# Kernel tuning notes

Hardware: AMD Instinct MI355X
Metric: run time of the kernel (lower is better)

Reference implementation:

```python
import jax, jax.numpy as jnp
import numpy as np

NUM_STEPS = 16  # step_index values in [0, 16); step 0 is excluded from pooling
BETA = 0.1
EPS = 1e-8


def setup_inputs() -> dict:
    key = jax.random.key(0)
    k1, k2, k3, k4, k5 = jax.random.split(key, 5)
    B, N, T, H, D = 8, 8, 2048, 2048, 1
    return {
        "policy_responses_logps": jax.random.normal(k1, (B, N, T, D), dtype=jnp.float32),
        "reference_responses_logps": jax.random.normal(k2, (B, N, T, D), dtype=jnp.float32),
        "hidden_state": jax.random.normal(k3, (B, N, T, H), dtype=jnp.float32),
        "step_index": jax.random.randint(k4, (B, N, T), 0, NUM_STEPS, dtype=jnp.int32),
        "labels": jax.random.normal(k5, (B, N), dtype=jnp.float32),
    }


def _segment_stats(onehot, x, counts):
    # onehot: [B,N,T,S], x: [B,N,T,F] -> per-step mean [B,N,S,F]
    ssum = jnp.einsum('bnts,bntf->bnsf', onehot, x)
    return ssum / jnp.maximum(counts, 1.0)[..., None]


def _lambda_rank_loss(pred, labels):
    # pred, labels: [B,N]
    N = pred.shape[1]
    diff = pred[:, :, None] - pred[:, None, :]            # [B,N,N]
    label_diff = labels[:, :, None] - labels[:, None, :]
    pairwise = -jax.nn.log_sigmoid(diff * jnp.sign(label_diff))
    return (pairwise.sum(axis=(1, 2)) / (N * (N - 1))).mean()


def reference(policy_responses_logps, reference_responses_logps, hidden_state, step_index, labels):
    logits = policy_responses_logps - reference_responses_logps  # [B,N,T,D]

    onehot = jax.nn.one_hot(step_index, NUM_STEPS, dtype=hidden_state.dtype)  # [B,N,T,S]
    counts = onehot.sum(axis=2)                                               # [B,N,S]

    step_hidden = _segment_stats(onehot, hidden_state, counts)  # [B,N,S,H]
    ref_hidden = step_hidden[:, 0:1]                             # [B,1,S,H]

    # cosine similarity between each (b,n,s) step-mean and the reference (n=0) step-mean
    dot = jnp.einsum('bnsh,bosh->bns', step_hidden, ref_hidden)
    nrm = jnp.maximum(jnp.linalg.norm(step_hidden, axis=-1), EPS)        # [B,N,S]
    ref_nrm = jnp.maximum(jnp.linalg.norm(ref_hidden, axis=-1), EPS)      # [B,1,S]
    cos = dot / (nrm * ref_nrm)

    s_ids = jnp.arange(NUM_STEPS)
    valid = (counts > 0) & (counts[:, 0:1] > 0) & (s_ids >= 1)[None, None, :]
    step_weights = jnp.where(valid, cos + 1.0, 0.0)                        # [B,N,S]

    step_logit = _segment_stats(onehot, logits, counts)                    # [B,N,S,D]
    weighted_sum = jnp.einsum('bns,bnsd->bnd', step_weights, step_logit)
    total_weight = step_weights.sum(axis=-1)                               # [B,N]
    weighted_logits = jnp.where(total_weight[..., None] > 0,
                                weighted_sum / jnp.maximum(total_weight, EPS)[..., None],
                                0.0)                                       # [B,N,D]

    text_logits = weighted_logits.mean(axis=-1)                            # [B,N]
    lr = _lambda_rank_loss(text_logits, labels)
    loss = -jax.nn.log_sigmoid(BETA * lr)

    chosen_rewards = (policy_responses_logps[:, 0, :] - reference_responses_logps[:, 0, :]).mean()
    rejected_rewards = (policy_responses_logps[:, -1, :] - reference_responses_logps[:, -1, :]).mean()
    return (loss, chosen_rewards, rejected_rewards)
```

## Files before the change

### kernel.cpp

```cpp
#include <hip/hip_runtime.h>
#include <math.h>

#define TT 2048
#define HH 2048
#define NSTEP 16
#define EPSF 1e-8f
#define BETA 0.1f
#define TSPLIT 2
#define TCHUNK (TT / TSPLIT)
#define ROW2 (HH / 2)
#define PART_FLOATS ((size_t)64 * NSTEP * HH)

typedef float f2v __attribute__((ext_vector_type(2)));

__global__ __launch_bounds__(256, 4) void k_segsum2(const float* __restrict__ hidden,
                                                    const int* __restrict__ step,
                                                    float2* __restrict__ part) {
  const int bn   = blockIdx.y;
  const int z    = blockIdx.z;
  const int col2 = blockIdx.x * 256 + threadIdx.x;
  const int t0   = z * TCHUNK;

  __shared__ int s_step[TCHUNK];
  for (int i = threadIdx.x; i < TCHUNK; i += 256) s_step[i] = step[bn * TT + t0 + i];
  __syncthreads();

  const f2v* hp = (const f2v*)hidden + (size_t)(bn * TT + t0) * ROW2 + col2;

  float2 acc[NSTEP];
#pragma unroll
  for (int k = 0; k < NSTEP; ++k) acc[k] = make_float2(0.f, 0.f);

  f2v va[8], vb[8];
  int4 sa0, sa1, sb0, sb1;

#define LOADS(S0, S1, base)                         \
  { S0 = *(const int4*)&s_step[(base)];             \
    S1 = *(const int4*)&s_step[(base) + 4]; }

#define LOADG(dst, base)                                        \
  _Pragma("unroll")                                             \
  for (int u = 0; u < 8; ++u)                                   \
    dst[u] = __builtin_nontemporal_load(&hp[(size_t)((base) + u) * ROW2]);

#define ACC1(V, SS)                                                            \
  { const int s_ = __builtin_amdgcn_readfirstlane(SS);                         \
    switch (s_) {                                                              \
      case 0:  acc[0].x  += V.x; acc[0].y  += V.y; break;                      \
      case 1:  acc[1].x  += V.x; acc[1].y  += V.y; break;                      \
      case 2:  acc[2].x  += V.x; acc[2].y  += V.y; break;                      \
      case 3:  acc[3].x  += V.x; acc[3].y  += V.y; break;                      \
      case 4:  acc[4].x  += V.x; acc[4].y  += V.y; break;                      \
      case 5:  acc[5].x  += V.x; acc[5].y  += V.y; break;                      \
      case 6:  acc[6].x  += V.x; acc[6].y  += V.y; break;                      \
      case 7:  acc[7].x  += V.x; acc[7].y  += V.y; break;                      \
      case 8:  acc[8].x  += V.x; acc[8].y  += V.y; break;                      \
      case 9:  acc[9].x  += V.x; acc[9].y  += V.y; break;                      \
      case 10: acc[10].x += V.x; acc[10].y += V.y; break;                      \
      case 11: acc[11].x += V.x; acc[11].y += V.y; break;                      \
      case 12: acc[12].x += V.x; acc[12].y += V.y; break;                      \
      case 13: acc[13].x += V.x; acc[13].y += V.y; break;                      \
      case 14: acc[14].x += V.x; acc[14].y += V.y; break;                      \
      case 15: acc[15].x += V.x; acc[15].y += V.y; break;                      \
    } }

#define PROC(src, S0, S1)                                                      \
  ACC1(src[0], S0.x) ACC1(src[1], S0.y) ACC1(src[2], S0.z) ACC1(src[3], S0.w) \
  ACC1(src[4], S1.x) ACC1(src[5], S1.y) ACC1(src[6], S1.z) ACC1(src[7], S1.w)

  LOADS(sa0, sa1, 0)
  LOADG(va, 0)
  for (int t = 0; t < TCHUNK; t += 16) {
    LOADS(sb0, sb1, t + 8)
    LOADG(vb, t + 8)
    PROC(va, sa0, sa1)
    if (t + 16 < TCHUNK) { LOADS(sa0, sa1, t + 16) LOADG(va, t + 16) }
    PROC(vb, sb0, sb1)
  }
#undef LOADS
#undef LOADG
#undef ACC1
#undef PROC

  float2* op = (float2*)part + (size_t)z * (PART_FLOATS / 2) +
               ((size_t)bn * NSTEP) * ROW2 + col2;
#pragma unroll
  for (int k = 0; k < NSTEP; ++k) op[(size_t)k * ROW2] = acc[k];
}

__global__ __launch_bounds__(1024) void k_bn(const float* __restrict__ pol,
                                             const float* __restrict__ refp,
                                             const int* __restrict__ step,
                                             const float* __restrict__ part,
                                             float* __restrict__ text_logits,
                                             float* __restrict__ out) {
  const int wave = threadIdx.x >> 6;
  const int lane = threadIdx.x & 63;

  if (blockIdx.x >= 64) {
    const int n = (blockIdx.x == 64) ? 0 : 7;
    __shared__ float red[16];
    const float4* p4 = (const float4*)pol;
    const float4* r4 = (const float4*)refp;
    float s = 0.f;
    for (int j = threadIdx.x; j < 4096; j += 1024) {
      const int b = j >> 9, t4 = j & 511;
      const int idx = (b * 8 + n) * 512 + t4;
      const float4 a = p4[idx], r = r4[idx];
      s += (a.x - r.x) + (a.y - r.y) + (a.z - r.z) + (a.w - r.w);
    }
#pragma unroll
    for (int off = 32; off > 0; off >>= 1) s += __shfl_down(s, off);
    if (lane == 0) red[wave] = s;
    __syncthreads();
    if (threadIdx.x == 0) {
      float tot = 0.f;
#pragma unroll
      for (int w = 0; w < 16; ++w) tot += red[w];
      out[(blockIdx.x == 64) ? 1 : 2] = tot / (8.f * TT);
    }
    return;
  }

  const int bn  = blockIdx.x;
  const int b   = bn >> 3;
  const int bn0 = b << 3;

  __shared__ float cnt_w[16][NSTEP], lsum_w[16][NSTEP], cnt0_w[16][NSTEP];
  __shared__ float cnt[NSTEP], cnt0[NSTEP], lsum[NSTEP], wgt[NSTEP];

  if (lane < NSTEP) {
    cnt_w[wave][lane] = 0.f; lsum_w[wave][lane] = 0.f; cnt0_w[wave][lane] = 0.f;
  }
  __syncthreads();

  for (int t = threadIdx.x; t < TT; t += 1024) {
    const int s = step[bn * TT + t];
    atomicAdd(&cnt_w[wave][s], 1.f);
    atomicAdd(&lsum_w[wave][s], pol[bn * TT + t] - refp[bn * TT + t]);
    const int s0 = step[bn0 * TT + t];
    atomicAdd(&cnt0_w[wave][s0], 1.f);
  }
  __syncthreads();

  if (threadIdx.x < NSTEP) {
    float c = 0.f, l = 0.f, c0 = 0.f;
#pragma unroll
    for (int w = 0; w < 16; ++w) {
      c  += cnt_w[w][threadIdx.x];
      l  += lsum_w[w][threadIdx.x];
      c0 += cnt0_w[w][threadIdx.x];
    }
    cnt[threadIdx.x] = c; lsum[threadIdx.x] = l; cnt0[threadIdx.x] = c0;
  }
  __syncthreads();

  const int s = wave;
  const float c  = fmaxf(cnt[s],  1.f);
  const float c0 = fmaxf(cnt0[s], 1.f);
  const float ic  = 1.f / c;
  const float ic0 = 1.f / c0;
  const float4* po0 = (const float4*)(part + ((size_t)bn  * NSTEP + s) * HH);
  const float4* po1 = (const float4*)(part + PART_FLOATS + ((size_t)bn  * NSTEP + s) * HH);
  const float4* pr0 = (const float4*)(part + ((size_t)bn0 * NSTEP + s) * HH);
  const float4* pr1 = (const float4*)(part + PART_FLOATS + ((size_t)bn0 * NSTEP + s) * HH);

  float dot = 0.f, nn = 0.f, rr = 0.f;
#pragma unroll
  for (int i = 0; i < 8; ++i) {
    const int idx = lane + i * 64;
    const float4 a0 = po0[idx], a1 = po1[idx];
    const float4 r0 = pr0[idx], r1 = pr1[idx];
    const float ax = (a0.x + a1.x) * ic,  ay = (a0.y + a1.y) * ic;
    const float az = (a0.z + a1.z) * ic,  aw = (a0.w + a1.w) * ic;
    const float rx = (r0.x + r1.x) * ic0, ry = (r0.y + r1.y) * ic0;
    const float rz = (r0.z + r1.z) * ic0, rw = (r0.w + r1.w) * ic0;
    dot += ax * rx + ay * ry + az * rz + aw * rw;
    nn  += ax * ax + ay * ay + az * az + aw * aw;
    rr  += rx * rx + ry * ry + rz * rz + rw * rw;
  }
#pragma unroll
  for (int off = 32; off > 0; off >>= 1) {
    dot += __shfl_down(dot, off);
    nn  += __shfl_down(nn,  off);
    rr  += __shfl_down(rr,  off);
  }
  if (lane == 0) {
    const float nrm = fmaxf(sqrtf(nn), EPSF);
    const float rn  = fmaxf(sqrtf(rr), EPSF);
    const float cosv = dot / (nrm * rn);
    const bool valid = (cnt[s] > 0.f) && (cnt0[s] > 0.f) && (s >= 1);
    wgt[s] = valid ? (cosv + 1.f) : 0.f;
  }
  __syncthreads();

  if (threadIdx.x == 0) {
    float wsum = 0.f, tw = 0.f;
#pragma unroll
    for (int k = 0; k < NSTEP; ++k) {
      const float w = wgt[k];
      wsum += w * (lsum[k] / fmaxf(cnt[k], 1.f));
      tw   += w;
    }
    text_logits[bn] = (tw > 0.f) ? (wsum / fmaxf(tw, EPSF)) : 0.f;
  }
}

__device__ inline float softplus_f(float x) {
  return fmaxf(x, 0.f) + log1pf(expf(-fabsf(x)));
}

__global__ __launch_bounds__(64) void k_final(const float* __restrict__ labels,
                                              const float* __restrict__ text_logits,
                                              float* __restrict__ out) {
  const int lane = threadIdx.x;
  float part = 0.f;
  {
    const int b = lane >> 3, i = lane & 7;
    const float pi = text_logits[b * 8 + i];
    const float li = labels[b * 8 + i];
#pragma unroll
    for (int j = 0; j < 8; ++j) {
      const float ld = li - labels[b * 8 + j];
      const float sg = (ld > 0.f) ? 1.f : ((ld < 0.f) ? -1.f : 0.f);
      const float z  = (pi - text_logits[b * 8 + j]) * sg;
      part += softplus_f(-z);
    }
  }
#pragma unroll
  for (int off = 32; off > 0; off >>= 1) part += __shfl_down(part, off);
  if (lane == 0) {
    const float lr = part / (56.f * 8.f);
    out[0] = softplus_f(-BETA * lr);
  }
}

extern "C" void kernel_launch(void* const* d_in, const int* in_sizes, int n_in,
                              void* d_out, int out_size, void* d_ws, size_t ws_size,
                              hipStream_t stream) {
  const float* pol    = (const float*)d_in[0];
  const float* refp   = (const float*)d_in[1];
  const float* hidden = (const float*)d_in[2];
  const int*   step   = (const int*)d_in[3];
  const float* labels = (const float*)d_in[4];
  float* out = (float*)d_out;

  float* part = (float*)d_ws;
  float* text_logits = part + (size_t)TSPLIT * PART_FLOATS;

  dim3 g1(4, 64, TSPLIT);
  k_segsum2<<<g1, 256, 0, stream>>>(hidden, step, (float2*)part);
  k_bn<<<66, 1024, 0, stream>>>(pol, refp, step, part, text_logits, out);
  k_final<<<1, 64, 0, stream>>>(labels, text_logits, out);
}
```

Baseline: 215.0 us.

## Use full-row 1024-thread blocks with four-way time split in segment-sum kernel

```diff
diff --git a/kernel.cpp b/kernel.cpp
--- a/kernel.cpp
+++ b/kernel.cpp
@@ -6,23 +6,23 @@
 #define NSTEP 16
 #define EPSF 1e-8f
 #define BETA 0.1f
-#define TSPLIT 2
+#define TSPLIT 4
 #define TCHUNK (TT / TSPLIT)
 #define ROW2 (HH / 2)
 #define PART_FLOATS ((size_t)64 * NSTEP * HH)
 
 typedef float f2v __attribute__((ext_vector_type(2)));
 
-__global__ __launch_bounds__(256, 4) void k_segsum2(const float* __restrict__ hidden,
-                                                    const int* __restrict__ step,
-                                                    float2* __restrict__ part) {
-  const int bn   = blockIdx.y;
-  const int z    = blockIdx.z;
-  const int col2 = blockIdx.x * 256 + threadIdx.x;
+__global__ __launch_bounds__(1024, 4) void k_segsum2(const float* __restrict__ hidden,
+                                                     const int* __restrict__ step,
+                                                     float2* __restrict__ part) {
+  const int bn   = blockIdx.x;
+  const int z    = blockIdx.y;
+  const int col2 = threadIdx.x;
   const int t0   = z * TCHUNK;
 
   __shared__ int s_step[TCHUNK];
-  for (int i = threadIdx.x; i < TCHUNK; i += 256) s_step[i] = step[bn * TT + t0 + i];
+  if (threadIdx.x < TCHUNK) s_step[threadIdx.x] = step[bn * TT + t0 + threadIdx.x];
   __syncthreads();
 
   const f2v* hp = (const f2v*)hidden + (size_t)(bn * TT + t0) * ROW2 + col2;
@@ -31,16 +31,14 @@
 #pragma unroll
   for (int k = 0; k < NSTEP; ++k) acc[k] = make_float2(0.f, 0.f);
 
-  f2v va[8], vb[8];
-  int4 sa0, sa1, sb0, sb1;
-
-#define LOADS(S0, S1, base)                         \
-  { S0 = *(const int4*)&s_step[(base)];             \
-    S1 = *(const int4*)&s_step[(base) + 4]; }
+  f2v va[4], vb[4];
+  int4 sa, sb;
+
+#define LOADS(S, base) { S = *(const int4*)&s_step[(base)]; }
 
 #define LOADG(dst, base)                                        \
   _Pragma("unroll")                                             \
-  for (int u = 0; u < 8; ++u)                                   \
+  for (int u = 0; u < 4; ++u)                                   \
     dst[u] = __builtin_nontemporal_load(&hp[(size_t)((base) + u) * ROW2]);
 
 #define ACC1(V, SS)                                                            \
@@ -64,18 +62,17 @@
       case 15: acc[15].x += V.x; acc[15].y += V.y; break;                      \
     } }
 
-#define PROC(src, S0, S1)                                                      \
-  ACC1(src[0], S0.x) ACC1(src[1], S0.y) ACC1(src[2], S0.z) ACC1(src[3], S0.w) \
-  ACC1(src[4], S1.x) ACC1(src[5], S1.y) ACC1(src[6], S1.z) ACC1(src[7], S1.w)
-
-  LOADS(sa0, sa1, 0)
+#define PROC(src, S)                                                           \
+  ACC1(src[0], S.x) ACC1(src[1], S.y) ACC1(src[2], S.z) ACC1(src[3], S.w)
+
+  LOADS(sa, 0)
   LOADG(va, 0)
-  for (int t = 0; t < TCHUNK; t += 16) {
-    LOADS(sb0, sb1, t + 8)
-    LOADG(vb, t + 8)
-    PROC(va, sa0, sa1)
-    if (t + 16 < TCHUNK) { LOADS(sa0, sa1, t + 16) LOADG(va, t + 16) }
-    PROC(vb, sb0, sb1)
+  for (int t = 0; t < TCHUNK; t += 8) {
+    LOADS(sb, t + 4)
+    LOADG(vb, t + 4)
+    PROC(va, sa)
+    if (t + 8 < TCHUNK) { LOADS(sa, t + 8) LOADG(va, t + 8) }
+    PROC(vb, sb)
   }
 #undef LOADS
 #undef LOADG
@@ -160,21 +157,24 @@
   const float c0 = fmaxf(cnt0[s], 1.f);
   const float ic  = 1.f / c;
   const float ic0 = 1.f / c0;
-  const float4* po0 = (const float4*)(part + ((size_t)bn  * NSTEP + s) * HH);
-  const float4* po1 = (const float4*)(part + PART_FLOATS + ((size_t)bn  * NSTEP + s) * HH);
-  const float4* pr0 = (const float4*)(part + ((size_t)bn0 * NSTEP + s) * HH);
-  const float4* pr1 = (const float4*)(part + PART_FLOATS + ((size_t)bn0 * NSTEP + s) * HH);
+  const size_t offA = ((size_t)bn  * NSTEP + s) * HH;
+  const size_t offR = ((size_t)bn0 * NSTEP + s) * HH;
 
   float dot = 0.f, nn = 0.f, rr = 0.f;
 #pragma unroll
   for (int i = 0; i < 8; ++i) {
     const int idx = lane + i * 64;
-    const float4 a0 = po0[idx], a1 = po1[idx];
-    const float4 r0 = pr0[idx], r1 = pr1[idx];
-    const float ax = (a0.x + a1.x) * ic,  ay = (a0.y + a1.y) * ic;
-    const float az = (a0.z + a1.z) * ic,  aw = (a0.w + a1.w) * ic;
-    const float rx = (r0.x + r1.x) * ic0, ry = (r0.y + r1.y) * ic0;
-    const float rz = (r0.z + r1.z) * ic0, rw = (r0.w + r1.w) * ic0;
+    float ax = 0.f, ay = 0.f, az = 0.f, aw = 0.f;
+    float rx = 0.f, ry = 0.f, rz = 0.f, rw = 0.f;
+#pragma unroll
+    for (int zz = 0; zz < TSPLIT; ++zz) {
+      const float4 a = ((const float4*)(part + (size_t)zz * PART_FLOATS + offA))[idx];
+      const float4 r = ((const float4*)(part + (size_t)zz * PART_FLOATS + offR))[idx];
+      ax += a.x; ay += a.y; az += a.z; aw += a.w;
+      rx += r.x; ry += r.y; rz += r.z; rw += r.w;
+    }
+    ax *= ic;  ay *= ic;  az *= ic;  aw *= ic;
+    rx *= ic0; ry *= ic0; rz *= ic0; rw *= ic0;
     dot += ax * rx + ay * ry + az * rz + aw * rw;
     nn  += ax * ax + ay * ay + az * az + aw * aw;
     rr  += rx * rx + ry * ry + rz * rz + rw * rw;
@@ -248,8 +248,8 @@
   float* part = (float*)d_ws;
   float* text_logits = part + (size_t)TSPLIT * PART_FLOATS;
 
-  dim3 g1(4, 64, TSPLIT);
-  k_segsum2<<<g1, 256, 0, stream>>>(hidden, step, (float2*)part);
+  dim3 g1(64, TSPLIT);
+  k_segsum2<<<g1, 1024, 0, stream>>>(hidden, step, (float2*)part);
   k_bn<<<66, 1024, 0, stream>>>(pol, refp, step, part, text_logits, out);
   k_final<<<1, 64, 0, stream>>>(labels, text_logits, out);
 }
```

Result: faster. 207.0 us (-3.7%).
